# Kernel tuning notes

Measured on AMD Instinct MI355X. Metric: run time of the kernel, lower is better.

Reference implementation:

```python
import jax, jax.numpy as jnp
import numpy as np

EPS = 1e-5


def setup_inputs() -> dict:
    key = jax.random.key(0)
    ks = jax.random.split(key, 8)
    g, p, d, h, w = 32, 64, 512, 24, 8
    hw = h * w
    return {
        "gal_fea": jax.random.normal(ks[0], (g, d, h, w), dtype=jnp.float32),
        "prob_fea": jax.random.normal(ks[1], (p, d, h, w), dtype=jnp.float32),
        "bn_weight": jnp.ones((1,), jnp.float32),
        "bn_bias": jnp.zeros((1,), jnp.float32),
        "bn_mean": jax.random.normal(ks[2], (1,), jnp.float32) * 0.1,
        "bn_var": jax.random.uniform(ks[3], (1,), jnp.float32, 0.5, 1.5),
        "fc_weight": jax.random.normal(ks[4], (1, 2 * hw), jnp.float32) * 0.05,
        "fc_bias": jnp.zeros((1,), jnp.float32),
        "lbn_weight": jnp.ones((1,), jnp.float32),
        "lbn_bias": jnp.zeros((1,), jnp.float32),
        "lbn_mean": jax.random.normal(ks[5], (1,), jnp.float32) * 0.1,
        "lbn_var": jax.random.uniform(ks[6], (1,), jnp.float32, 0.5, 1.5),
    }


def reference(gal_fea, prob_fea, bn_weight, bn_bias, bn_mean, bn_var,
              fc_weight, fc_bias, lbn_weight, lbn_bias, lbn_mean, lbn_var):
    g, d, h, w = gal_fea.shape
    p = prob_fea.shape[0]
    hw = h * w
    # 1x1 conv with probe pixels as kernels == batched correlation (QK^T style)
    gal = gal_fea.reshape(g, d, hw)                                  # [g, d, hw_x]
    ker = jnp.transpose(prob_fea, (0, 2, 3, 1)).reshape(p, hw, d)    # [p, hw_y, d]
    s = jnp.einsum('gdx,pyd->gpyx', gal, ker)                        # [g, p, hw_y, hw_x]
    # dual-axis max pooling, then concat: [g, p, 2*hw]
    score = jnp.concatenate([s.max(axis=2), s.max(axis=3)], axis=-1)
    # BatchNorm1d(1) in eval mode: scalar affine with running stats
    score = (score - bn_mean) * (bn_weight / jnp.sqrt(bn_var + EPS)) + bn_bias
    # fc: Linear(2*hw, 1)
    score = score.reshape(g * p, 2 * hw) @ fc_weight[0] + fc_bias[0]  # [g*p]
    score = score.reshape(g, p)
    # logit BatchNorm1d(1), eval mode
    score = (score - lbn_mean) * (lbn_weight / jnp.sqrt(lbn_var + EPS)) + lbn_bias
    return jax.nn.sigmoid(score / 10.0)
```

## Files before the change

### kernel.cpp

```cpp
#include <hip/hip_runtime.h>
#include <hip/hip_bf16.h>
#include <cstdint>
#include <cstddef>

#define NG 32
#define NP 64
#define ND 512
#define HW 192
#define EPSV 1e-5f

typedef _Float16 half8 __attribute__((ext_vector_type(8)));
typedef float floatx4 __attribute__((ext_vector_type(4)));
typedef float floatx16 __attribute__((ext_vector_type(16)));

__global__ __launch_bounds__(192) void prep_probe(const float* __restrict__ prob,
                                                  _Float16* __restrict__ probT2) {
  const int p = blockIdx.x, s = blockIdx.y;
  const int r = threadIdx.x;
  const float* src = prob + ((size_t)p * ND + s * 8) * HW + r;
  half8 h;
#pragma unroll
  for (int j = 0; j < 8; ++j) h[j] = (_Float16)src[(size_t)j * HW];
  *(half8*)(probT2 + (((size_t)p * 64 + s) * HW + r) * 8) = h;
}

__global__ __launch_bounds__(256) void prep_gal(const float* __restrict__ gal,
                                                _Float16* __restrict__ galT) {
  __shared__ float tile[32][33];
  const int zg = blockIdx.z;
  const float* sp = gal + (size_t)zg * ND * HW;
  _Float16* dp = galT + (size_t)zg * HW * ND;
  const int k0 = blockIdx.x * 32, s0 = blockIdx.y * 32;
  const int tx = threadIdx.x & 31, ty = threadIdx.x >> 5;
#pragma unroll
  for (int i = ty; i < 32; i += 8)
    tile[i][tx] = sp[(size_t)(k0 + i) * HW + s0 + tx];
  __syncthreads();
#pragma unroll
  for (int i = ty; i < 32; i += 8)
    dp[(size_t)(s0 + i) * ND + k0 + tx] = (_Float16)tile[tx][i];
}

__device__ __forceinline__ void g2l16(const void* g, void* l) {
  __builtin_amdgcn_global_load_lds(
      (const __attribute__((address_space(1))) void*)g,
      (__attribute__((address_space(3))) void*)l, 16, 0, 0);
}

__global__ __launch_bounds__(256, 2) void qaconv_main(
    const _Float16* __restrict__ galT, const _Float16* __restrict__ probT2,
    const float* __restrict__ bn_w, const float* __restrict__ bn_b,
    const float* __restrict__ bn_m, const float* __restrict__ bn_v,
    const float* __restrict__ fc_w, const float* __restrict__ fc_b,
    const float* __restrict__ lbn_w, const float* __restrict__ lbn_b,
    const float* __restrict__ lbn_m, const float* __restrict__ lbn_v,
    float* __restrict__ out) {
  __shared__ __align__(16) char shmem[50688];
  __shared__ float colp[2][HW];
  __shared__ float wsum[4];
  char* bufB = shmem;
  float(*rowbuf)[66] = (float(*)[66])shmem;

  const int bid = blockIdx.x;
  const int g = bid >> 6, p = bid & 63;
  const int t = threadIdx.x;
  const int lane = t & 63, wid = t >> 6;
  const int wr = wid & 1;
  const int wc = wid >> 1;
  const int l31 = lane & 31, hi = lane >> 5;
  const int arow0 = wr * 96 + l31;

  const _Float16* aBase = probT2 + (((size_t)p * 64 + hi) * HW + arow0) * 8;

  const int srow = t >> 3;
  const int sswz = (t & 7) ^ (srow & 7);
  const _Float16* gBl = galT + (size_t)g * HW * ND + (size_t)srow * ND + sswz * 8;

  floatx16 acc[3][3];
#pragma unroll
  for (int i = 0; i < 3; ++i)
#pragma unroll
    for (int j = 0; j < 3; ++j) acc[i][j] = (floatx16)0.f;

#define STAGE_B(kt_, buf_)                                          \
  {                                                                 \
    char* db_ = bufB + (buf_)*24576 + wid * 1024;                   \
    const _Float16* sb_ = gBl + (size_t)(kt_)*64;                   \
    _Pragma("unroll") for (int r6 = 0; r6 < 6; ++r6)                \
        g2l16(sb_ + (size_t)r6 * 32 * ND, db_ + r6 * 4096);         \
  }

#define LOAD_AF(dst, idx_)                                          \
  {                                                                 \
    const _Float16* ap_ = aBase + (size_t)(idx_) * (2 * HW * 8);    \
    dst[0] = *(const half8*)(ap_);                                  \
    dst[1] = *(const half8*)(ap_ + 32 * 8);                         \
    dst[2] = *(const half8*)(ap_ + 64 * 8);                         \
  }

#define KC_BODY(kc_, AFU, AFL, nidx_)                                            \
  {                                                                              \
    LOAD_AF(AFL, nidx_);                                                         \
    half8 bf[3];                                                                 \
    const int sl_ = (kc_)*2 + hi;                                                \
    const int swz_ = (sl_ ^ (l31 & 7)) << 4;                                     \
    _Pragma("unroll") for (int f = 0; f < 3; ++f) {                              \
      const int rb_ = wc * 96 + f * 32 + l31;                                    \
      bf[f] = *(const half8*)(bcur + rb_ * 128 + swz_);                          \
    }                                                                            \
    __builtin_amdgcn_s_setprio(1);                                               \
    _Pragma("unroll") for (int i = 0; i < 3; ++i)                                \
        _Pragma("unroll") for (int j = 0; j < 3; ++j)                            \
            acc[i][j] = __builtin_amdgcn_mfma_f32_32x32x16_f16(AFU[i], bf[j],    \
                                                               acc[i][j], 0, 0, 0); \
    __builtin_amdgcn_s_setprio(0);                                               \
  }

  half8 af0[3], af1[3];
  STAGE_B(0, 0);
  LOAD_AF(af0, 0);
  __syncthreads();

  for (int kt = 0; kt < 8; ++kt) {
    if (kt < 7) STAGE_B(kt + 1, (kt & 1) ^ 1);
    const char* bcur = bufB + (kt & 1) * 24576;
    const int i0 = kt * 4;
    const int n4 = (kt < 7) ? i0 + 4 : 31;
    KC_BODY(0, af0, af1, i0 + 1)
    KC_BODY(1, af1, af0, i0 + 2)
    KC_BODY(2, af0, af1, i0 + 3)
    KC_BODY(3, af1, af0, n4)
    __syncthreads();
  }

#pragma unroll
  for (int fb = 0; fb < 3; ++fb) {
    float v = -3.4e38f;
#pragma unroll
    for (int fa = 0; fa < 3; ++fa)
#pragma unroll
      for (int e = 0; e < 16; ++e) v = fmaxf(v, acc[fa][fb][e]);
    v = fmaxf(v, __shfl_xor(v, 32));
    if (lane < 32) colp[wr][wc * 96 + fb * 32 + lane] = v;
  }
#pragma unroll
  for (int fa = 0; fa < 3; ++fa)
#pragma unroll
    for (int e = 0; e < 16; ++e) {
      float rv = acc[fa][0][e];
      rv = fmaxf(rv, acc[fa][1][e]);
      rv = fmaxf(rv, acc[fa][2][e]);
      const int Y = wr * 96 + fa * 32 + (e & 3) + 8 * (e >> 2) + 4 * hi;
      rowbuf[Y][wc * 32 + l31] = rv;
    }
  __syncthreads();

  float partial = 0.f;
  if (t < HW) {
    const float* rb = rowbuf[t];
    float rmax = -3.4e38f;
#pragma unroll
    for (int j = 0; j < 16; ++j) {
      const floatx4 v = *(const floatx4*)&rb[j * 4];
      rmax = fmaxf(rmax, fmaxf(fmaxf(v[0], v[1]), fmaxf(v[2], v[3])));
    }
    const float cmax = fmaxf(colp[0][t], colp[1][t]);
    const float scale = bn_w[0] / sqrtf(bn_v[0] + EPSV);
    const float bm = bn_m[0], bb = bn_b[0];
    partial = ((cmax - bm) * scale + bb) * fc_w[t] +
              ((rmax - bm) * scale + bb) * fc_w[HW + t];
  }
#pragma unroll
  for (int off = 1; off < 64; off <<= 1) partial += __shfl_xor(partial, off);
  if (lane == 0) wsum[wid] = partial;
  __syncthreads();
  if (t == 0) {
    const float sum = fc_b[0] + wsum[0] + wsum[1] + wsum[2] + wsum[3];
    const float logit = (sum - lbn_m[0]) * (lbn_w[0] / sqrtf(lbn_v[0] + EPSV)) + lbn_b[0];
    out[bid] = 1.f / (1.f + expf(-logit * 0.1f));
  }
#undef STAGE_B
#undef LOAD_AF
#undef KC_BODY
}

__global__ __launch_bounds__(256) void qaconv_naive(
    const float* __restrict__ gal, const float* __restrict__ prob,
    const float* __restrict__ bn_w, const float* __restrict__ bn_b,
    const float* __restrict__ bn_m, const float* __restrict__ bn_v,
    const float* __restrict__ fc_w, const float* __restrict__ fc_b,
    const float* __restrict__ lbn_w, const float* __restrict__ lbn_b,
    const float* __restrict__ lbn_m, const float* __restrict__ lbn_v,
    float* __restrict__ out) {
  __shared__ float prow[ND];
  __shared__ float rowmaxs[HW];
  __shared__ float colmaxs[HW];
  __shared__ float red[4];
  const int bid = blockIdx.x;
  const int g = bid >> 6, p = bid & 63;
  const int t = threadIdx.x, lane = t & 63, wid = t >> 6;
  const float* gp = gal + (size_t)g * ND * HW;
  const float* pp = prob + (size_t)p * ND * HW;
  float colmax = -3.4e38f;
  for (int y = 0; y < HW; ++y) {
    for (int k = t; k < ND; k += 256) prow[k] = pp[(size_t)k * HW + y];
    __syncthreads();
    float sv = -3.4e38f;
    if (t < HW) {
      sv = 0.f;
      for (int k = 0; k < ND; ++k) sv = fmaf(prow[k], gp[(size_t)k * HW + t], sv);
      colmax = fmaxf(colmax, sv);
    }
    float m = sv;
#pragma unroll
    for (int off = 1; off < 64; off <<= 1) m = fmaxf(m, __shfl_xor(m, off));
    if (lane == 0) red[wid] = m;
    __syncthreads();
    if (t == 0) rowmaxs[y] = fmaxf(fmaxf(red[0], red[1]), fmaxf(red[2], red[3]));
    __syncthreads();
  }
  if (t < HW) colmaxs[t] = colmax;
  __syncthreads();
  float partial = 0.f;
  for (int j = t; j < 2 * HW; j += 256) {
    const float v = (j < HW) ? colmaxs[j] : rowmaxs[j - HW];
    const float sc = (v - bn_m[0]) * (bn_w[0] / sqrtf(bn_v[0] + EPSV)) + bn_b[0];
    partial += sc * fc_w[j];
  }
#pragma unroll
  for (int off = 1; off < 64; off <<= 1) partial += __shfl_xor(partial, off);
  if (lane == 0) red[wid] = partial;
  __syncthreads();
  if (t == 0) {
    const float sum = fc_b[0] + red[0] + red[1] + red[2] + red[3];
    const float logit = (sum - lbn_m[0]) * (lbn_w[0] / sqrtf(lbn_v[0] + EPSV)) + lbn_b[0];
    out[bid] = 1.f / (1.f + expf(-logit * 0.1f));
  }
}

extern "C" void kernel_launch(void* const* d_in, const int* in_sizes, int n_in,
                              void* d_out, int out_size, void* d_ws, size_t ws_size,
                              hipStream_t stream) {
  const float* gal = (const float*)d_in[0];
  const float* prob = (const float*)d_in[1];
  const float* bn_w = (const float*)d_in[2];
  const float* bn_b = (const float*)d_in[3];
  const float* bn_m = (const float*)d_in[4];
  const float* bn_v = (const float*)d_in[5];
  const float* fc_w = (const float*)d_in[6];
  const float* fc_b = (const float*)d_in[7];
  const float* lbn_w = (const float*)d_in[8];
  const float* lbn_b = (const float*)d_in[9];
  const float* lbn_m = (const float*)d_in[10];
  const float* lbn_v = (const float*)d_in[11];
  float* out = (float*)d_out;

  const size_t probT2_elems = (size_t)NP * 64 * HW * 8;
  const size_t galT_elems = (size_t)NG * HW * ND;
  const size_t ws_needed = (probT2_elems + galT_elems) * sizeof(_Float16);
  if (ws_size >= ws_needed) {
    _Float16* probT2 = (_Float16*)d_ws;
    _Float16* galT = probT2 + probT2_elems;
    prep_probe<<<dim3(NP, 64), dim3(192), 0, stream>>>(prob, probT2);
    prep_gal<<<dim3(16, 6, NG), dim3(256), 0, stream>>>(gal, galT);
    qaconv_main<<<dim3(NG * NP), dim3(256), 0, stream>>>(
        galT, probT2, bn_w, bn_b, bn_m, bn_v, fc_w, fc_b, lbn_w, lbn_b, lbn_m, lbn_v, out);
  } else {
    qaconv_naive<<<dim3(NG * NP), dim3(256), 0, stream>>>(
        gal, prob, bn_w, bn_b, bn_m, bn_v, fc_w, fc_b, lbn_w, lbn_b, lbn_m, lbn_v, out);
  }
}
```

Before: 94.58 us.

## Remap block order for L2 locality, relayout gallery LDS tiles, relax loop barrier

Block indices are remapped so that blocks sharing a probe land on the same XCD group and gallery reuse stays in cache. The staged gallery tile in LDS is rearranged to a plain row-contiguous layout per 32-row slab, which drops the XOR swizzle arithmetic on reads. The end-of-iteration __syncthreads is replaced by a partial vmcnt wait plus s_barrier, with a sched_barrier added after staging. The partial vmcnt wait may not cover every outstanding LDS-direct load, and the new LDS layout could introduce bank conflicts.

```diff
diff --git a/kernel.cpp b/kernel.cpp
--- a/kernel.cpp
+++ b/kernel.cpp
@@ -61,8 +61,11 @@
   char* bufB = shmem;
   float(*rowbuf)[66] = (float(*)[66])shmem;
 
-  const int bid = blockIdx.x;
-  const int g = bid >> 6, p = bid & 63;
+  const int i = blockIdx.x;
+  const int L = (i & 7) * 256 + (i >> 3);
+  const int p = (L >> 8) * 8 + ((L & 255) >> 5);
+  const int g = L & 31;
+
   const int t = threadIdx.x;
   const int lane = t & 63, wid = t >> 6;
   const int wr = wid & 1;
@@ -72,22 +75,21 @@
 
   const _Float16* aBase = probT2 + (((size_t)p * 64 + hi) * HW + arow0) * 8;
 
-  const int srow = t >> 3;
-  const int sswz = (t & 7) ^ (srow & 7);
-  const _Float16* gBl = galT + (size_t)g * HW * ND + (size_t)srow * ND + sswz * 8;
+  const _Float16* gBl = galT + (size_t)g * HW * ND + (size_t)(t & 31) * ND + ((t >> 5) & 7) * 8;
+  const int sdst = wid * 1024;
 
   floatx16 acc[3][3];
 #pragma unroll
-  for (int i = 0; i < 3; ++i)
-#pragma unroll
-    for (int j = 0; j < 3; ++j) acc[i][j] = (floatx16)0.f;
+  for (int ii = 0; ii < 3; ++ii)
+#pragma unroll
+    for (int jj = 0; jj < 3; ++jj) acc[ii][jj] = (floatx16)0.f;
 
 #define STAGE_B(kt_, buf_)                                          \
   {                                                                 \
-    char* db_ = bufB + (buf_)*24576 + wid * 1024;                   \
+    char* db_ = bufB + (buf_)*24576 + sdst;                         \
     const _Float16* sb_ = gBl + (size_t)(kt_)*64;                   \
-    _Pragma("unroll") for (int r6 = 0; r6 < 6; ++r6)                \
-        g2l16(sb_ + (size_t)r6 * 32 * ND, db_ + r6 * 4096);         \
+    _Pragma("unroll") for (int r_ = 0; r_ < 6; ++r_)                \
+        g2l16(sb_ + (size_t)r_ * 32 * ND, db_ + r_ * 4096);         \
   }
 
 #define LOAD_AF(dst, idx_)                                          \
@@ -102,17 +104,15 @@
   {                                                                              \
     LOAD_AF(AFL, nidx_);                                                         \
     half8 bf[3];                                                                 \
-    const int sl_ = (kc_)*2 + hi;                                                \
-    const int swz_ = (sl_ ^ (l31 & 7)) << 4;                                     \
-    _Pragma("unroll") for (int f = 0; f < 3; ++f) {                              \
-      const int rb_ = wc * 96 + f * 32 + l31;                                    \
-      bf[f] = *(const half8*)(bcur + rb_ * 128 + swz_);                          \
-    }                                                                            \
+    const int boff_ = ((kc_)*2 + hi) * 512 + l31 * 16;                           \
+    bf[0] = *(const half8*)(bcur + (wc * 3 + 0) * 4096 + boff_);                 \
+    bf[1] = *(const half8*)(bcur + (wc * 3 + 1) * 4096 + boff_);                 \
+    bf[2] = *(const half8*)(bcur + (wc * 3 + 2) * 4096 + boff_);                 \
     __builtin_amdgcn_s_setprio(1);                                               \
-    _Pragma("unroll") for (int i = 0; i < 3; ++i)                                \
-        _Pragma("unroll") for (int j = 0; j < 3; ++j)                            \
-            acc[i][j] = __builtin_amdgcn_mfma_f32_32x32x16_f16(AFU[i], bf[j],    \
-                                                               acc[i][j], 0, 0, 0); \
+    _Pragma("unroll") for (int ii = 0; ii < 3; ++ii)                             \
+        _Pragma("unroll") for (int jj = 0; jj < 3; ++jj)                         \
+            acc[ii][jj] = __builtin_amdgcn_mfma_f32_32x32x16_f16(AFU[ii], bf[jj],\
+                                                                 acc[ii][jj], 0, 0, 0); \
     __builtin_amdgcn_s_setprio(0);                                               \
   }
 
@@ -123,6 +123,7 @@
 
   for (int kt = 0; kt < 8; ++kt) {
     if (kt < 7) STAGE_B(kt + 1, (kt & 1) ^ 1);
+    __builtin_amdgcn_sched_barrier(0x10F);
     const char* bcur = bufB + (kt & 1) * 24576;
     const int i0 = kt * 4;
     const int n4 = (kt < 7) ? i0 + 4 : 31;
@@ -130,7 +131,8 @@
     KC_BODY(1, af1, af0, i0 + 2)
     KC_BODY(2, af0, af1, i0 + 3)
     KC_BODY(3, af1, af0, n4)
-    __syncthreads();
+    asm volatile("s_waitcnt vmcnt(3)" ::: "memory");
+    __builtin_amdgcn_s_barrier();
   }
 
 #pragma unroll
@@ -177,7 +179,7 @@
   if (t == 0) {
     const float sum = fc_b[0] + wsum[0] + wsum[1] + wsum[2] + wsum[3];
     const float logit = (sum - lbn_m[0]) * (lbn_w[0] / sqrtf(lbn_v[0] + EPSV)) + lbn_b[0];
-    out[bid] = 1.f / (1.f + expf(-logit * 0.1f));
+    out[g * NP + p] = 1.f / (1.f + expf(-logit * 0.1f));
   }
 #undef STAGE_B
 #undef LOAD_AF
```

New measurement: 111.8 us. +18.2%, slower.
